# Kernel optimization log

Measured on AMD Instinct MI355X. Metric: run time of the kernel, lower is better.

Reference implementation:

```python
import jax, jax.numpy as jnp
import numpy as np
from jax import lax

WS = 8        # window size
SHIFT = 4     # window_size // 2, applied because depth=1 is odd
HEADS = 6
DIM = 192


def setup_inputs() -> dict:
    key = jax.random.key(0)
    k0, k1, k2, k3 = jax.random.split(key, 4)
    x = jax.random.normal(k0, (4, DIM, 256, 256), jnp.float32)
    qkv_w = jax.random.normal(k1, (3 * DIM, DIM), jnp.float32) * 0.05   # 1x1 conv weight (squeezed)
    dw_w = jax.random.normal(k2, (3 * DIM, 1, 3, 3), jnp.float32) * 0.05  # depthwise 3x3, groups=3*DIM
    proj_w = jax.random.normal(k3, (DIM, DIM), jnp.float32) * 0.05      # project_out 1x1
    temperature = jnp.ones((HEADS, 1, 1), jnp.float32)
    return {"x": x, "qkv_w": qkv_w, "dw_w": dw_w, "proj_w": proj_w,
            "temperature": temperature}


def _l2norm(t):
    # matches torch F.normalize(dim=-1, eps=1e-12)
    n = jnp.sqrt(jnp.sum(t * t, axis=-1, keepdims=True))
    return t / jnp.maximum(n, 1e-12)


def reference(x, qkv_w, dw_w, proj_w, temperature):
    b, c, h, w = x.shape
    # shifted-window roll (depth odd)
    x = jnp.roll(x, (-SHIFT, -SHIFT), axis=(2, 3))
    nh, nw = h // WS, w // WS
    # window partition: (b, c, h, w) -> (b*nh*nw, c, WS, WS)
    xw = x.reshape(b, c, nh, WS, nw, WS).transpose(0, 2, 4, 1, 3, 5)
    xw = xw.reshape(b * nh * nw, c, WS, WS)
    # qkv 1x1 conv then depthwise 3x3 conv (padding=1), applied per-window
    qkv = jnp.einsum('oc,bchw->bohw', qkv_w, xw)
    qkv = lax.conv_general_dilated(
        qkv, dw_w, window_strides=(1, 1), padding='SAME',
        feature_group_count=3 * c,
        dimension_numbers=('NCHW', 'OIHW', 'NCHW'))
    q, k, v = jnp.split(qkv, 3, axis=1)
    B = q.shape[0]
    cph = c // HEADS
    to_heads = lambda t: t.reshape(B, HEADS, cph, WS * WS)  # b head c (hw)
    q, k, v = to_heads(q), to_heads(k), to_heads(v)
    q = _l2norm(q)
    k = _l2norm(k)
    # channel-wise (transposed) attention: [B, head, cph, cph]
    attn = jnp.einsum('bhcn,bhdn->bhcd', q, k) * temperature[None]
    attn = jax.nn.softmax(attn, axis=-1)
    out = jnp.einsum('bhcd,bhdn->bhcn', attn, v)
    out = out.reshape(B, c, WS, WS)
    # window reverse
    out = out.reshape(b, nh, nw, c, WS, WS).transpose(0, 3, 1, 4, 2, 5)
    out = out.reshape(b, c, h, w)
    out = jnp.einsum('oc,bchw->bohw', proj_w, out)
    out = jnp.roll(out, (SHIFT, SHIFT), axis=(2, 3))
    return out
```

## Files before the change

kernel.cpp:

```cpp
#include <hip/hip_runtime.h>
#include <math.h>

typedef short bf16x8 __attribute__((ext_vector_type(8)));
typedef float floatx4 __attribute__((ext_vector_type(4)));

#define NC 192
#define HH 256
#define WSZ 8
#define NSHIFT 4
#define NHEADS 6

#define QKVH_STRIDE 68
#define ATTN_STRIDE 36
#define OBUF_STRIDE 36
#define OBUF_OFF 26112
#define FRAG_OFF 35328
#define LDS_TOTAL 49664

#define QKV_FRAG_ELEMS (576 * 192)

__device__ __forceinline__ unsigned short f2bf(float f) {
    union { float f; unsigned int u; } v; v.f = f;
    unsigned int u = v.u + 0x7FFFu + ((v.u >> 16) & 1u);
    return (unsigned short)(u >> 16);
}

__global__ void preproc_kernel(const float* __restrict__ qkv_w,
                               const float* __restrict__ proj_w,
                               unsigned short* __restrict__ ws) {
    int e = blockIdx.x * 256 + threadIdx.x;
    if (e < QKV_FRAG_ELEMS) {
        int blk = e >> 9, l = (e >> 3) & 63, j = e & 7;
        int mt = blk / 6, kt = blk % 6;
        ws[e] = f2bf(qkv_w[(mt * 16 + (l & 15)) * NC + kt * 32 + (l >> 4) * 8 + j]);
    } else if (e < QKV_FRAG_ELEMS + NC * NC) {
        int e2 = e - QKV_FRAG_ELEMS;
        int blk = e2 >> 9, l = (e2 >> 3) & 63, j = e2 & 7;
        int mt = blk / 6, kt = blk % 6;
        ws[e] = f2bf(proj_w[(mt * 16 + (l & 15)) * NC + kt * 32 + (l >> 4) * 8 + j]);
    }
}

__global__ __launch_bounds__(256, 3) void attn_main(
    const float* __restrict__ x, const unsigned short* __restrict__ wsA,
    const float* __restrict__ dw_w, const float* __restrict__ temperature,
    float* __restrict__ out)
{
    __shared__ __align__(16) unsigned char smem[LDS_TOTAL];
    float* qkvh = (float*)smem;
    unsigned short* xstage = (unsigned short*)smem;
    float* attnb = (float*)smem;
    float* obuf  = (float*)(smem + OBUF_OFF);
    unsigned short* frags = (unsigned short*)(smem + FRAG_OFF);

    const int t = threadIdx.x;
    const int lane = t & 63;
    const int wv = t >> 6;
    const int quad = lane >> 4;
    const int l15 = lane & 15;
    const int blk = blockIdx.x;
    const int b = blk >> 10, wi = (blk >> 5) & 31, wj = blk & 31;

    for (int idx = t; idx < NC * 16; idx += 256) {
        int c = idx >> 4, r = (idx >> 1) & 7, s4 = idx & 1;
        int hh = (wi * WSZ + r + NSHIFT) & 255;
        int ww = (wj * WSZ + s4 * 4 + NSHIFT) & 255;
        float4 v4 = *((const float4*)(x + ((size_t)(b * NC + c) * HH + hh) * HH + ww));
        int kt = c >> 5, ko = c & 31;
        int p0 = r * 8 + s4 * 4;
        int fr = kt * 4 + (p0 >> 4);
        int lxb = ((ko >> 3) << 4) | (p0 & 15);
        unsigned short* dst = xstage + (fr * 64 + lxb) * 8 + (ko & 7);
        dst[0]  = f2bf(v4.x);
        dst[8]  = f2bf(v4.y);
        dst[16] = f2bf(v4.z);
        dst[24] = f2bf(v4.w);
    }
    __syncthreads();

    bf16x8 Bx[6];
    #pragma unroll
    for (int kt = 0; kt < 6; ++kt)
        Bx[kt] = *((const bf16x8*)(xstage + ((kt * 4 + wv) * 64 + lane) * 8));
    __syncthreads();

    bf16x8 pB0, pB1, pB2, pB3, pB4, pB5;

    #pragma unroll 1
    for (int h = 0; h < NHEADS; ++h) {
        #pragma unroll
        for (int mtl = 0; mtl < 6; ++mtl) {
            int part = mtl >> 1, sub = mtl & 1;
            int mt_g = part * 12 + h * 2 + sub;
            const bf16x8* aptr = (const bf16x8*)wsA + (size_t)(mt_g * 6) * 64 + lane;
            floatx4 acc = {0.f, 0.f, 0.f, 0.f};
            #pragma unroll
            for (int kt = 0; kt < 6; ++kt) {
                bf16x8 a = aptr[kt * 64];
                acc = __builtin_amdgcn_mfma_f32_16x16x32_bf16(a, Bx[kt], acc, 0, 0, 0);
            }
            int rowbase = part * 32 + sub * 16 + quad * 4;
            int col = wv * 16 + l15;
            #pragma unroll
            for (int rg = 0; rg < 4; ++rg)
                qkvh[(rowbase + rg) * QKVH_STRIDE + col] = acc[rg];
        }
        __syncthreads();

        if (t < 192) {
            int ch = t >> 1, half = t & 1;
            int part = ch >> 5;
            int g = part * NC + h * 32 + (ch & 31);
            const float* wp = dw_w + (size_t)g * 9;
            float w[9];
            #pragma unroll
            for (int i = 0; i < 9; ++i) w[i] = wp[i];
            const float* base = qkvh + ch * QKVH_STRIDE;
            int r0 = half * 4;
            float dwout[4][8];
            float ra[8], rb[8], rc[8];
            auto loadrow = [&](float* dst, int r2) {
                if ((unsigned)r2 < 8u) {
                    float4 lo = *((const float4*)(base + r2 * 8));
                    float4 hi = *((const float4*)(base + r2 * 8 + 4));
                    dst[0]=lo.x; dst[1]=lo.y; dst[2]=lo.z; dst[3]=lo.w;
                    dst[4]=hi.x; dst[5]=hi.y; dst[6]=hi.z; dst[7]=hi.w;
                } else {
                    #pragma unroll
                    for (int i = 0; i < 8; ++i) dst[i] = 0.f;
                }
            };
            auto conv3 = [&](float* o, const float* rm, const float* rz, const float* rp) {
                #pragma unroll
                for (int s = 0; s < 8; ++s) {
                    float acc = w[1]*rm[s] + w[4]*rz[s] + w[7]*rp[s];
                    if (s > 0) acc += w[0]*rm[s-1] + w[3]*rz[s-1] + w[6]*rp[s-1];
                    if (s < 7) acc += w[2]*rm[s+1] + w[5]*rz[s+1] + w[8]*rp[s+1];
                    o[s] = acc;
                }
            };
            loadrow(ra, r0 - 1); loadrow(rb, r0); loadrow(rc, r0 + 1);
            conv3(dwout[0], ra, rb, rc);
            loadrow(ra, r0 + 2); conv3(dwout[1], rb, rc, ra);
            loadrow(rb, r0 + 3); conv3(dwout[2], rc, ra, rb);
            loadrow(rc, r0 + 4); conv3(dwout[3], ra, rb, rc);

            float ss = 0.f;
            #pragma unroll
            for (int ro = 0; ro < 4; ++ro)
                #pragma unroll
                for (int s = 0; s < 8; ++s) ss += dwout[ro][s] * dwout[ro][s];
            ss += __shfl_xor(ss, 1, 64);
            float sc = 1.0f / fmaxf(sqrtf(ss), 1e-12f);

            if (part < 2) {
                int mt = (ch & 31) >> 4;
                int fid = part * 4 + mt * 2 + half;
                unsigned short* fb = frags + fid * 512 + (ch & 15) * 8;
                #pragma unroll
                for (int ro = 0; ro < 4; ++ro) {
                    bf16x8 o;
                    #pragma unroll
                    for (int s = 0; s < 8; ++s) o[s] = (short)f2bf(dwout[ro][s] * sc);
                    *((bf16x8*)(fb + ro * 128)) = o;
                }
            } else {
                int chv = ch & 31;
                int quad_t = chv >> 3, j = chv & 7;
                #pragma unroll
                for (int ro = 0; ro < 4; ++ro) {
                    int fid = 8 + half * 2 + (ro >> 1);
                    int l15b = (ro & 1) * 8;
                    unsigned short* fb = frags + fid * 512 + ((quad_t << 4) | l15b) * 8 + j;
                    #pragma unroll
                    for (int s = 0; s < 8; ++s)
                        fb[s * 8] = f2bf(dwout[ro][s]);
                }
            }
        }
        __syncthreads();

        {
            int mt = wv >> 1, ntk = wv & 1;
            floatx4 acc = {0.f, 0.f, 0.f, 0.f};
            #pragma unroll
            for (int kt = 0; kt < 2; ++kt) {
                bf16x8 aq = *((const bf16x8*)(frags + (mt * 2 + kt) * 512 + lane * 8));
                bf16x8 bk = *((const bf16x8*)(frags + (4 + ntk * 2 + kt) * 512 + lane * 8));
                acc = __builtin_amdgcn_mfma_f32_16x16x32_bf16(aq, bk, acc, 0, 0, 0);
            }
            float tmp = temperature[h];
            #pragma unroll
            for (int rg = 0; rg < 4; ++rg)
                attnb[(mt * 16 + quad * 4 + rg) * ATTN_STRIDE + ntk * 16 + l15] = acc[rg] * tmp;
        }
        __syncthreads();

        if (t < 128) {
            int row = t >> 2, sl = t & 3;
            const float* src = attnb + row * ATTN_STRIDE + sl * 8;
            float4 lo = *((const float4*)src), hi = *((const float4*)(src + 4));
            float v[8] = {lo.x, lo.y, lo.z, lo.w, hi.x, hi.y, hi.z, hi.w};
            float mx = v[0];
            #pragma unroll
            for (int i = 1; i < 8; ++i) mx = fmaxf(mx, v[i]);
            mx = fmaxf(mx, __shfl_xor(mx, 1, 64));
            mx = fmaxf(mx, __shfl_xor(mx, 2, 64));
            float sum = 0.f;
            #pragma unroll
            for (int i = 0; i < 8; ++i) { v[i] = __expf(v[i] - mx); sum += v[i]; }
            sum += __shfl_xor(sum, 1, 64);
            sum += __shfl_xor(sum, 2, 64);
            float inv = 1.0f / sum;
            bf16x8 o;
            #pragma unroll
            for (int i = 0; i < 8; ++i) o[i] = (short)f2bf(v[i] * inv);
            *((bf16x8*)(frags + (12 + (row >> 4)) * 512 + (sl * 16 + (row & 15)) * 8)) = o;
        }
        __syncthreads();

        {
            bf16x8 bv = *((const bf16x8*)(frags + (8 + wv) * 512 + lane * 8));
            #pragma unroll
            for (int mt = 0; mt < 2; ++mt) {
                bf16x8 aa = *((const bf16x8*)(frags + (12 + mt) * 512 + lane * 8));
                floatx4 acc = {0.f, 0.f, 0.f, 0.f};
                acc = __builtin_amdgcn_mfma_f32_16x16x32_bf16(aa, bv, acc, 0, 0, 0);
                #pragma unroll
                for (int rg = 0; rg < 4; ++rg)
                    obuf[(wv * 16 + l15) * OBUF_STRIDE + mt * 16 + quad * 4 + rg] = acc[rg];
            }
        }
        __syncthreads();

        {
            const float* src = obuf + (wv * 16 + l15) * OBUF_STRIDE + quad * 8;
            float4 lo = *((const float4*)src), hi = *((const float4*)(src + 4));
            float v[8] = {lo.x, lo.y, lo.z, lo.w, hi.x, hi.y, hi.z, hi.w};
            bf16x8 o;
            #pragma unroll
            for (int i = 0; i < 8; ++i) o[i] = (short)f2bf(v[i]);
            switch (h) {
                case 0: pB0 = o; break;
                case 1: pB1 = o; break;
                case 2: pB2 = o; break;
                case 3: pB3 = o; break;
                case 4: pB4 = o; break;
                default: pB5 = o; break;
            }
        }
    }

    const bf16x8* apro = (const bf16x8*)(wsA + QKV_FRAG_ELEMS);
    int px = wv * 16 + l15;
    int r = px >> 3, s = px & 7;
    int hh = (wi * WSZ + r + NSHIFT) & 255;
    int ww = (wj * WSZ + s + NSHIFT) & 255;
    #pragma unroll
    for (int mt = 0; mt < 12; ++mt) {
        const bf16x8* ap = apro + (size_t)(mt * 6) * 64 + lane;
        floatx4 acc = {0.f, 0.f, 0.f, 0.f};
        acc = __builtin_amdgcn_mfma_f32_16x16x32_bf16(ap[0 * 64], pB0, acc, 0, 0, 0);
        acc = __builtin_amdgcn_mfma_f32_16x16x32_bf16(ap[1 * 64], pB1, acc, 0, 0, 0);
        acc = __builtin_amdgcn_mfma_f32_16x16x32_bf16(ap[2 * 64], pB2, acc, 0, 0, 0);
        acc = __builtin_amdgcn_mfma_f32_16x16x32_bf16(ap[3 * 64], pB3, acc, 0, 0, 0);
        acc = __builtin_amdgcn_mfma_f32_16x16x32_bf16(ap[4 * 64], pB4, acc, 0, 0, 0);
        acc = __builtin_amdgcn_mfma_f32_16x16x32_bf16(ap[5 * 64], pB5, acc, 0, 0, 0);
        int chb = mt * 16 + quad * 4;
        #pragma unroll
        for (int rg = 0; rg < 4; ++rg)
            out[((size_t)(b * NC + chb + rg) * HH + hh) * HH + ww] = acc[rg];
    }
}

extern "C" void kernel_launch(void* const* d_in, const int* in_sizes, int n_in,
                              void* d_out, int out_size, void* d_ws, size_t ws_size,
                              hipStream_t stream) {
    const float* x           = (const float*)d_in[0];
    const float* qkv_w       = (const float*)d_in[1];
    const float* dw_w        = (const float*)d_in[2];
    const float* proj_w      = (const float*)d_in[3];
    const float* temperature = (const float*)d_in[4];
    float* out = (float*)d_out;
    unsigned short* wsA = (unsigned short*)d_ws;

    int total = QKV_FRAG_ELEMS + NC * NC;
    hipLaunchKernelGGL(preproc_kernel, dim3((total + 255) / 256), dim3(256), 0, stream,
                       qkv_w, proj_w, wsA);
    hipLaunchKernelGGL(attn_main, dim3(4 * 32 * 32), dim3(256), 0, stream,
                       x, wsA, dw_w, temperature, out);
}
```

Before: 681.4 us.

## Swizzle LDS layouts, shrink shared memory, drop a sync, raise occupancy

Adds XOR and rotation swizzles to the LDS staging of x, the qkv tile, the q/k fragments and the attention fragments to cut bank conflicts. V is now written back as fp32 into qkvh and packed into bf16 fragments by each wave. The per-head output goes straight to bf16 in a buffer that overlays the fragment region, which removes one barrier. The input loads pair two channels and pack them into 32-bit writes. Lower LDS use allows launch bounds of 4 blocks per CU, at the cost of register pressure and more intricate index maths.

```diff
diff --git a/kernel.cpp b/kernel.cpp
--- a/kernel.cpp
+++ b/kernel.cpp
@@ -12,10 +12,9 @@
 
 #define QKVH_STRIDE 68
 #define ATTN_STRIDE 36
-#define OBUF_STRIDE 36
-#define OBUF_OFF 26112
-#define FRAG_OFF 35328
-#define LDS_TOTAL 49664
+#define OB_STRIDE 40
+#define FRAG_OFF 26112
+#define LDS_TOTAL 40448
 
 #define QKV_FRAG_ELEMS (576 * 192)
 
@@ -23,6 +22,10 @@
     union { float f; unsigned int u; } v; v.f = f;
     unsigned int u = v.u + 0x7FFFu + ((v.u >> 16) & 1u);
     return (unsigned short)(u >> 16);
+}
+
+__device__ __forceinline__ unsigned int pk2(float a, float b) {
+    return (unsigned int)f2bf(a) | ((unsigned int)f2bf(b) << 16);
 }
 
 __global__ void preproc_kernel(const float* __restrict__ qkv_w,
@@ -41,7 +44,7 @@
     }
 }
 
-__global__ __launch_bounds__(256, 3) void attn_main(
+__global__ __launch_bounds__(256, 4) void attn_main(
     const float* __restrict__ x, const unsigned short* __restrict__ wsA,
     const float* __restrict__ dw_w, const float* __restrict__ temperature,
     float* __restrict__ out)
@@ -50,8 +53,8 @@
     float* qkvh = (float*)smem;
     unsigned short* xstage = (unsigned short*)smem;
     float* attnb = (float*)smem;
-    float* obuf  = (float*)(smem + OBUF_OFF);
     unsigned short* frags = (unsigned short*)(smem + FRAG_OFF);
+    unsigned short* obw   = (unsigned short*)(smem + FRAG_OFF);
 
     const int t = threadIdx.x;
     const int lane = t & 63;
@@ -61,27 +64,35 @@
     const int blk = blockIdx.x;
     const int b = blk >> 10, wi = (blk >> 5) & 31, wj = blk & 31;
 
-    for (int idx = t; idx < NC * 16; idx += 256) {
-        int c = idx >> 4, r = (idx >> 1) & 7, s4 = idx & 1;
+    for (int idx = t; idx < (NC / 2) * 16; idx += 256) {
+        int c2 = idx >> 4;
+        int c = c2 * 2;
+        int r = (idx >> 1) & 7, s4 = idx & 1;
         int hh = (wi * WSZ + r + NSHIFT) & 255;
         int ww = (wj * WSZ + s4 * 4 + NSHIFT) & 255;
-        float4 v4 = *((const float4*)(x + ((size_t)(b * NC + c) * HH + hh) * HH + ww));
+        const float* xb = x + ((size_t)(b * NC + c) * HH + hh) * HH + ww;
+        float4 v0 = *((const float4*)xb);
+        float4 v1 = *((const float4*)(xb + (size_t)HH * HH));
         int kt = c >> 5, ko = c & 31;
         int p0 = r * 8 + s4 * 4;
         int fr = kt * 4 + (p0 >> 4);
-        int lxb = ((ko >> 3) << 4) | (p0 & 15);
-        unsigned short* dst = xstage + (fr * 64 + lxb) * 8 + (ko & 7);
-        dst[0]  = f2bf(v4.x);
-        dst[8]  = f2bf(v4.y);
-        dst[16] = f2bf(v4.z);
-        dst[24] = f2bf(v4.w);
+        int lxb0 = ((ko >> 3) << 4) | (p0 & 15);
+        int m = r & 3;
+        unsigned int* dstb = (unsigned int*)xstage + (fr * 64 + lxb0) * 4 + ((ko & 7) >> 1);
+        dstb[(0 ^ m) * 4] = pk2(v0.x, v1.x);
+        dstb[(1 ^ m) * 4] = pk2(v0.y, v1.y);
+        dstb[(2 ^ m) * 4] = pk2(v0.z, v1.z);
+        dstb[(3 ^ m) * 4] = pk2(v0.w, v1.w);
     }
     __syncthreads();
 
     bf16x8 Bx[6];
-    #pragma unroll
-    for (int kt = 0; kt < 6; ++kt)
-        Bx[kt] = *((const bf16x8*)(xstage + ((kt * 4 + wv) * 64 + lane) * 8));
+    {
+        int bxor = ((wv & 1) << 1) | ((lane >> 3) & 1);
+        #pragma unroll
+        for (int kt = 0; kt < 6; ++kt)
+            Bx[kt] = *((const bf16x8*)(xstage + ((kt * 4 + wv) * 64 + (lane ^ bxor)) * 8));
+    }
     __syncthreads();
 
     bf16x8 pB0, pB1, pB2, pB3, pB4, pB5;
@@ -100,10 +111,10 @@
                 acc = __builtin_amdgcn_mfma_f32_16x16x32_bf16(a, Bx[kt], acc, 0, 0, 0);
             }
             int rowbase = part * 32 + sub * 16 + quad * 4;
-            int col = wv * 16 + l15;
+            int colp = ((wv * 16 + l15) + (((rowbase >> 3) & 3) << 4)) & 63;
             #pragma unroll
             for (int rg = 0; rg < 4; ++rg)
-                qkvh[(rowbase + rg) * QKVH_STRIDE + col] = acc[rg];
+                qkvh[(rowbase + rg) * QKVH_STRIDE + colp] = acc[rg];
         }
         __syncthreads();
 
@@ -116,13 +127,14 @@
             #pragma unroll
             for (int i = 0; i < 9; ++i) w[i] = wp[i];
             const float* base = qkvh + ch * QKVH_STRIDE;
+            int sw16 = ((ch >> 3) & 3) << 4;
             int r0 = half * 4;
             float dwout[4][8];
             float ra[8], rb[8], rc[8];
             auto loadrow = [&](float* dst, int r2) {
                 if ((unsigned)r2 < 8u) {
-                    float4 lo = *((const float4*)(base + r2 * 8));
-                    float4 hi = *((const float4*)(base + r2 * 8 + 4));
+                    float4 lo = *((const float4*)(base + ((r2 * 8 + sw16) & 63)));
+                    float4 hi = *((const float4*)(base + ((r2 * 8 + 4 + sw16) & 63)));
                     dst[0]=lo.x; dst[1]=lo.y; dst[2]=lo.z; dst[3]=lo.w;
                     dst[4]=hi.x; dst[5]=hi.y; dst[6]=hi.z; dst[7]=hi.w;
                 } else {
@@ -145,18 +157,18 @@
             loadrow(rb, r0 + 3); conv3(dwout[2], rc, ra, rb);
             loadrow(rc, r0 + 4); conv3(dwout[3], ra, rb, rc);
 
-            float ss = 0.f;
-            #pragma unroll
-            for (int ro = 0; ro < 4; ++ro)
+            if (part < 2) {
+                float ss = 0.f;
                 #pragma unroll
-                for (int s = 0; s < 8; ++s) ss += dwout[ro][s] * dwout[ro][s];
-            ss += __shfl_xor(ss, 1, 64);
-            float sc = 1.0f / fmaxf(sqrtf(ss), 1e-12f);
-
-            if (part < 2) {
+                for (int ro = 0; ro < 4; ++ro)
+                    #pragma unroll
+                    for (int s = 0; s < 8; ++s) ss += dwout[ro][s] * dwout[ro][s];
+                ss += __shfl_xor(ss, 1, 64);
+                float sc = 1.0f / fmaxf(sqrtf(ss), 1e-12f);
                 int mt = (ch & 31) >> 4;
                 int fid = part * 4 + mt * 2 + half;
-                unsigned short* fb = frags + fid * 512 + (ch & 15) * 8;
+                int x2 = fid & 3;
+                unsigned short* fb = frags + fid * 512 + ((ch & 15) ^ x2) * 8;
                 #pragma unroll
                 for (int ro = 0; ro < 4; ++ro) {
                     bf16x8 o;
@@ -165,16 +177,12 @@
                     *((bf16x8*)(fb + ro * 128)) = o;
                 }
             } else {
-                int chv = ch & 31;
-                int quad_t = chv >> 3, j = chv & 7;
+                float* dst = qkvh + ch * QKVH_STRIDE;
                 #pragma unroll
                 for (int ro = 0; ro < 4; ++ro) {
-                    int fid = 8 + half * 2 + (ro >> 1);
-                    int l15b = (ro & 1) * 8;
-                    unsigned short* fb = frags + fid * 512 + ((quad_t << 4) | l15b) * 8 + j;
-                    #pragma unroll
-                    for (int s = 0; s < 8; ++s)
-                        fb[s * 8] = f2bf(dwout[ro][s]);
+                    int c0 = (r0 + ro) * 8;
+                    *((float4*)(dst + ((c0 + sw16) & 63)))     = make_float4(dwout[ro][0], dwout[ro][1], dwout[ro][2], dwout[ro][3]);
+                    *((float4*)(dst + ((c0 + 4 + sw16) & 63))) = make_float4(dwout[ro][4], dwout[ro][5], dwout[ro][6], dwout[ro][7]);
                 }
             }
         }
@@ -185,14 +193,25 @@
             floatx4 acc = {0.f, 0.f, 0.f, 0.f};
             #pragma unroll
             for (int kt = 0; kt < 2; ++kt) {
-                bf16x8 aq = *((const bf16x8*)(frags + (mt * 2 + kt) * 512 + lane * 8));
-                bf16x8 bk = *((const bf16x8*)(frags + (4 + ntk * 2 + kt) * 512 + lane * 8));
+                int fq = mt * 2 + kt, fk = ntk * 2 + kt;
+                bf16x8 aq = *((const bf16x8*)(frags + fq * 512 + (lane ^ (fq & 3)) * 8));
+                bf16x8 bk = *((const bf16x8*)(frags + (4 + fk) * 512 + (lane ^ (fk & 3)) * 8));
                 acc = __builtin_amdgcn_mfma_f32_16x16x32_bf16(aq, bk, acc, 0, 0, 0);
             }
             float tmp = temperature[h];
             #pragma unroll
             for (int rg = 0; rg < 4; ++rg)
                 attnb[(mt * 16 + quad * 4 + rg) * ATTN_STRIDE + ntk * 16 + l15] = acc[rg] * tmp;
+        }
+        {
+            int px = wv * 16 + l15;
+            int chb = 64 + quad * 8;
+            int colp = (px + (quad << 4)) & 63;
+            bf16x8 o;
+            #pragma unroll
+            for (int j = 0; j < 8; ++j)
+                o[j] = (short)f2bf(qkvh[(chb + j) * QKVH_STRIDE + colp]);
+            *((bf16x8*)(frags + (8 + wv) * 512 + lane * 8)) = o;
         }
         __syncthreads();
 
@@ -215,31 +234,25 @@
             bf16x8 o;
             #pragma unroll
             for (int i = 0; i < 8; ++i) o[i] = (short)f2bf(v[i] * inv);
-            *((bf16x8*)(frags + (12 + (row >> 4)) * 512 + (sl * 16 + (row & 15)) * 8)) = o;
+            *((bf16x8*)(frags + (12 + (row >> 4)) * 512 + (sl * 16 + ((row & 15) ^ sl)) * 8)) = o;
         }
         __syncthreads();
 
         {
             bf16x8 bv = *((const bf16x8*)(frags + (8 + wv) * 512 + lane * 8));
+            int axor = (lane >> 4) & 3;
             #pragma unroll
             for (int mt = 0; mt < 2; ++mt) {
-                bf16x8 aa = *((const bf16x8*)(frags + (12 + mt) * 512 + lane * 8));
+                bf16x8 aa = *((const bf16x8*)(frags + (12 + mt) * 512 + (lane ^ axor) * 8));
                 floatx4 acc = {0.f, 0.f, 0.f, 0.f};
                 acc = __builtin_amdgcn_mfma_f32_16x16x32_bf16(aa, bv, acc, 0, 0, 0);
-                #pragma unroll
-                for (int rg = 0; rg < 4; ++rg)
-                    obuf[(wv * 16 + l15) * OBUF_STRIDE + mt * 16 + quad * 4 + rg] = acc[rg];
-            }
-        }
-        __syncthreads();
-
+                int uidx = (wv * 16 + l15) * OB_STRIDE + mt * 16 + quad * 4;
+                *((uint2*)((unsigned int*)obw + (uidx >> 1))) =
+                    make_uint2(pk2(acc[0], acc[1]), pk2(acc[2], acc[3]));
+            }
+        }
         {
-            const float* src = obuf + (wv * 16 + l15) * OBUF_STRIDE + quad * 8;
-            float4 lo = *((const float4*)src), hi = *((const float4*)(src + 4));
-            float v[8] = {lo.x, lo.y, lo.z, lo.w, hi.x, hi.y, hi.z, hi.w};
-            bf16x8 o;
-            #pragma unroll
-            for (int i = 0; i < 8; ++i) o[i] = (short)f2bf(v[i]);
+            bf16x8 o = *((const bf16x8*)(obw + (wv * 16 + l15) * OB_STRIDE + quad * 8));
             switch (h) {
                 case 0: pB0 = o; break;
                 case 1: pB1 = o; break;
```

Result: slower. 997.1 us (+46.3%).
